# Optimization experiments

Hardware: AMD Instinct MI355X
Metric: run time of the kernel (lower is better)

Reference implementation:

```python
import jax, jax.numpy as jnp
import numpy as np

ALPHA = 0.2  # LeakyReLU negative slope
NEG_INF = -9e15


def setup_inputs() -> dict:
    key = jax.random.key(0)
    k1, k2, k3, k4 = jax.random.split(key, 4)
    B, N, F_in, F_out = 8, 2048, 256, 128
    x = jax.random.normal(k1, (B, N, F_in), dtype=jnp.float32)
    adj = jax.random.randint(k2, (B, N, N), 0, 2, dtype=jnp.int32)
    # xavier-uniform-like init
    limW = float(np.sqrt(6.0 / (F_in + F_out)))
    W = jax.random.uniform(k3, (F_in, F_out), jnp.float32, -limW, limW)
    lima = float(np.sqrt(6.0 / (2 * F_out + 1)))
    a = jax.random.uniform(k4, (2 * F_out, 1), jnp.float32, -lima, lima)
    return {"x": x, "adj": adj, "W": W, "a": a}


def reference(x, adj, W, a):
    # x: [B, N, F_in], adj: [B, N, N], W: [F_in, F_out], a: [2*F_out, 1]
    F_out = W.shape[1]
    h = jnp.einsum('bnf,fo->bno', x, W)            # [B, N, F_out]
    a1 = a[:F_out, 0]                               # attends to source node i
    a2 = a[F_out:, 0]                               # attends to target node j
    f1 = h @ a1                                     # [B, N]
    f2 = h @ a2                                     # [B, N]
    # e[b,i,j] = leakyrelu(a1.h_i + a2.h_j) -- factored form of the concat trick
    e = jax.nn.leaky_relu(f1[:, :, None] + f2[:, None, :], negative_slope=ALPHA)
    attention = jnp.where(adj > 0, e, NEG_INF)
    attention = jax.nn.softmax(attention, axis=2)   # [B, N, N]
    # dropout is identity in eval mode
    h_prime = jnp.einsum('bij,bjo->bio', attention, h)  # [B, N, F_out]
    return jax.nn.elu(h_prime)                      # concat=True -> ELU
```

## Files before the change

### kernel.cpp

```cpp
#include <hip/hip_runtime.h>
#include <stdint.h>

#define BB   8
#define NN   2048
#define FIN  256
#define FOUT 128

using short8 = __attribute__((ext_vector_type(8))) short;
using f32x4  = __attribute__((ext_vector_type(4))) float;

__device__ __forceinline__ unsigned short rbf(float f) {
    return (unsigned short)((__float_as_uint(f) + 0x8000u) >> 16);
}

__device__ __forceinline__ void mfma_calib(int m, int quad, int* Mlab, int* Nlab) {
    short8 pa1, pb1, pa2, pb2;
    const short one = (short)0x3F80;
    const short mb  = (short)rbf((float)m);
#pragma unroll
    for (int j = 0; j < 8; ++j) { pa1[j] = 0; pa2[j] = 0; pb1[j] = mb; pb2[j] = one; }
    if (quad == 0) { pa1[0] = one; pa2[0] = mb; }
    f32x4 zz = {0.f, 0.f, 0.f, 0.f};
    f32x4 c1 = __builtin_amdgcn_mfma_f32_16x16x32_bf16(pa1, pb1, zz, 0, 0, 0);
    f32x4 c2 = __builtin_amdgcn_mfma_f32_16x16x32_bf16(pa2, pb2, zz, 0, 0, 0);
#pragma unroll
    for (int r = 0; r < 4; ++r) {
        Nlab[r] = ((int)c1[r]) & 15;
        Mlab[r] = ((int)c2[r]) & 15;
    }
}

__global__ __launch_bounds__(256) void gat_wt(const float* __restrict__ W,
                                              unsigned short* __restrict__ wt) {
    const int g  = blockIdx.x * 256 + threadIdx.x;
    const int k  = g >> 5;
    const int o4 = (g & 31) << 2;
    float4 wv = *(const float4*)(W + (k << 7) + o4);
    wt[((o4 + 0) << 8) + k] = rbf(wv.x);
    wt[((o4 + 1) << 8) + k] = rbf(wv.y);
    wt[((o4 + 2) << 8) + k] = rbf(wv.z);
    wt[((o4 + 3) << 8) + k] = rbf(wv.w);
}

__global__ __launch_bounds__(256) void gat_bm2(const int* __restrict__ adj,
                                               unsigned char* __restrict__ bm) {
    const int row = blockIdx.x;
    const int tid = threadIdx.x;
    const int4* p = (const int4*)(adj + ((size_t)row << 11) + (tid << 3));
    int4 a0 = p[0];
    int4 a1 = p[1];
    unsigned int b = (unsigned int)(a0.x > 0)
                   | ((unsigned int)(a0.y > 0) << 1)
                   | ((unsigned int)(a0.z > 0) << 2)
                   | ((unsigned int)(a0.w > 0) << 3)
                   | ((unsigned int)(a1.x > 0) << 4)
                   | ((unsigned int)(a1.y > 0) << 5)
                   | ((unsigned int)(a1.z > 0) << 6)
                   | ((unsigned int)(a1.w > 0) << 7);
    const int w = tid >> 6, c = (tid >> 2) & 15, q = tid & 3;
    bm[((size_t)(row >> 5) << 13) + (c << 9) + (w << 7) + (q << 5) + (row & 31)]
        = (unsigned char)b;
}

__global__ __launch_bounds__(256) void gat_h4(
        const float* __restrict__ x, const unsigned short* __restrict__ wt,
        const float* __restrict__ a, unsigned short* __restrict__ ht,
        float* __restrict__ f1, float* __restrict__ f2) {
    __shared__ unsigned short xs[16][264];
    __shared__ float hs[16][132];
    const int bk   = blockIdx.x;
    const int R0   = bk << 4;
    const int b    = R0 >> 11;
    const int il0  = R0 & (NN - 1);
    const int tid  = threadIdx.x;
    const int w    = tid >> 6;
    const int lane = tid & 63;
    const int m    = lane & 15;
    const int quad = lane >> 4;

#pragma unroll
    for (int rr = 0; rr < 4; ++rr) {
        const int row = (w << 2) + rr;
        float4 xv = *(const float4*)(x + (size_t)(R0 + row) * FIN + (lane << 2));
        ushort4 c4;
        c4.x = rbf(xv.x); c4.y = rbf(xv.y); c4.z = rbf(xv.z); c4.w = rbf(xv.w);
        *(ushort4*)(&xs[row][lane << 2]) = c4;
    }
    int Mlab[4], Nlab[4];
    mfma_calib(m, quad, Mlab, Nlab);
    __syncthreads();

    f32x4 zz = {0.f, 0.f, 0.f, 0.f};
    f32x4 acc[2] = {zz, zz};
#pragma unroll
    for (int kc = 0; kc < 8; ++kc) {
        const int k0 = (kc << 5) + (quad << 3);
        short8 av = *(const short8*)(&xs[m][k0]);
#pragma unroll
        for (int t = 0; t < 2; ++t) {
            const int ot = (w << 1) + t;
            short8 bw = *(const short8*)(wt + (((ot << 4) + m) << 8) + k0);
            acc[t] = __builtin_amdgcn_mfma_f32_16x16x32_bf16(av, bw, acc[t], 0, 0, 0);
        }
    }
#pragma unroll
    for (int t = 0; t < 2; ++t)
#pragma unroll
        for (int r = 0; r < 4; ++r)
            hs[Mlab[r]][(((w << 1) + t) << 4) + Nlab[r]] = acc[t][r];
    __syncthreads();

    {
        const int i   = tid >> 4;
        const int seg = tid & 15;
        const int o0  = seg << 3;
        float s1 = 0.f, s2 = 0.f;
#pragma unroll
        for (int e = 0; e < 8; ++e) {
            float hv = hs[i][o0 + e];
            s1 = fmaf(hv, a[o0 + e], s1);
            s2 = fmaf(hv, a[FOUT + o0 + e], s2);
        }
        s1 += __shfl_xor(s1, 1); s1 += __shfl_xor(s1, 2);
        s1 += __shfl_xor(s1, 4); s1 += __shfl_xor(s1, 8);
        s2 += __shfl_xor(s2, 1); s2 += __shfl_xor(s2, 2);
        s2 += __shfl_xor(s2, 4); s2 += __shfl_xor(s2, 8);
        if (seg == 0) { f1[R0 + i] = s1; f2[R0 + i] = s2; }
    }
    {
        const int o  = tid >> 1;
        const int i8 = (tid & 1) << 3;
        const int jj = il0 + i8;
        const int wj = jj >> 9;
        const int cj = (jj >> 5) & 15;
        const int qj = (jj >> 3) & 3;
        short8 hv;
#pragma unroll
        for (int e = 0; e < 8; ++e) hv[e] = (short)rbf(hs[i8 + e][o]);
        const size_t addr = ((size_t)b << 18) + ((size_t)wj << 16) + (cj << 12)
                          + ((o >> 4) << 9) + (((qj << 4) + (o & 15)) << 3);
        *(short8*)(ht + addr) = hv;
    }
}

#define LOADC(H, MskA, MskB, Fa, Fb, c) { \
    const unsigned short* hp_ = htb + ((c) << 12); \
    _Pragma("unroll") \
    for (int ot = 0; ot < 8; ++ot) \
        H[ot] = *(const short8*)(hp_ + (ot << 9) + (lane << 3)); \
    MskA = bmb[((c) << 9) + mq]; \
    MskB = bmb[((c) << 9) + mq + 16]; \
    const int j0_ = jb + ((c) << 5); \
    Fa = *(const float4*)(f2b + j0_); \
    Fb = *(const float4*)(f2b + j0_ + 4); \
}

#define COMPC(H, MskA, MskB, Fa, Fb) { \
    float fm_[8] = {Fa.x, Fa.y, Fa.z, Fa.w, Fb.x, Fb.y, Fb.z, Fb.w}; \
    float pA_[8], pB_[8]; \
    _Pragma("unroll") \
    for (int u = 0; u < 8; ++u) { \
        float e = f1a + fm_[u]; \
        pA_[u] = (MskA & (1u << u)) ? __expf(fmaxf(e, 0.2f * e)) : 0.f; \
    } \
    _Pragma("unroll") \
    for (int u = 0; u < 8; ++u) { \
        float e = f1b + fm_[u]; \
        pB_[u] = (MskB & (1u << u)) ? __expf(fmaxf(e, 0.2f * e)) : 0.f; \
    } \
    s1 += ((pA_[0]+pA_[1])+(pA_[2]+pA_[3]))+((pA_[4]+pA_[5])+(pA_[6]+pA_[7])); \
    s2 += ((pB_[0]+pB_[1])+(pB_[2]+pB_[3]))+((pB_[4]+pB_[5])+(pB_[6]+pB_[7])); \
    short8 pf1_, pf2_; \
    _Pragma("unroll") \
    for (int u = 0; u < 8; ++u) { pf1_[u] = (short)rbf(pA_[u]); pf2_[u] = (short)rbf(pB_[u]); } \
    _Pragma("unroll") \
    for (int ot = 0; ot < 8; ++ot) { \
        acc1[ot] = __builtin_amdgcn_mfma_f32_16x16x32_bf16(pf1_, H[ot], acc1[ot], 0, 0, 0); \
        acc2[ot] = __builtin_amdgcn_mfma_f32_16x16x32_bf16(pf2_, H[ot], acc2[ot], 0, 0, 0); \
    } \
}

__global__ __launch_bounds__(256, 2) void gat_s6(
        const unsigned char* __restrict__ bm, const unsigned short* __restrict__ ht,
        const float* __restrict__ f1, const float* __restrict__ f2,
        float* __restrict__ out) {
    const int bk   = blockIdx.x;
    const int b    = bk & 7;
    const int i0   = (bk >> 3) << 5;
    const int tid  = threadIdx.x;
    const int w    = tid >> 6;
    const int lane = tid & 63;
    const int m    = lane & 15;
    const int quad = lane >> 4;

    __shared__ float accb[2][32][128];
    __shared__ float sbuf[4][2][16];

    const int gi0 = (b << 11) + i0;
    const float f1a = f1[gi0 + m];
    const float f1b = f1[gi0 + 16 + m];
    const unsigned char* bmb = bm + ((size_t)gi0 << 8);
    const int mq = (w << 7) + (quad << 5) + m;
    const float* f2b = f2 + (b << 11);
    const unsigned short* htb = ht + ((size_t)b << 18) + ((size_t)w << 16);

    const int jb  = (w << 9) + (quad << 3);

    f32x4 zz = {0.f, 0.f, 0.f, 0.f};
    f32x4 acc1[8], acc2[8];
#pragma unroll
    for (int t = 0; t < 8; ++t) { acc1[t] = zz; acc2[t] = zz; }
    float s1 = 0.f, s2 = 0.f;

    short8 hfA[8], hfB[8];
    unsigned int mA0, mB0, mA1, mB1;
    float4 faA, fbA, faB, fbB;

    LOADC(hfA, mA0, mB0, faA, fbA, 0);
    for (int cc = 0; cc < 7; ++cc) {
        const int c0 = cc << 1;
        LOADC(hfB, mA1, mB1, faB, fbB, c0 + 1);
        COMPC(hfA, mA0, mB0, faA, fbA);
        LOADC(hfA, mA0, mB0, faA, fbA, c0 + 2);
        COMPC(hfB, mA1, mB1, faB, fbB);
    }
    LOADC(hfB, mA1, mB1, faB, fbB, 15);
    COMPC(hfA, mA0, mB0, faA, fbA);
    COMPC(hfB, mA1, mB1, faB, fbB);

    s1 += __shfl_xor(s1, 16); s1 += __shfl_xor(s1, 32);
    s2 += __shfl_xor(s2, 16); s2 += __shfl_xor(s2, 32);
    if (lane < 16) { sbuf[w][0][lane] = s1; sbuf[w][1][lane] = s2; }

    int Mlab[4], Nlab[4];
    mfma_calib(m, quad, Mlab, Nlab);

    if (w < 2) {
#pragma unroll
        for (int ot = 0; ot < 8; ++ot)
#pragma unroll
            for (int r = 0; r < 4; ++r) {
                accb[w][Mlab[r]][(ot << 4) + Nlab[r]]      = acc1[ot][r];
                accb[w][16 + Mlab[r]][(ot << 4) + Nlab[r]] = acc2[ot][r];
            }
    }
    __syncthreads();
    if (w >= 2) {
#pragma unroll
        for (int ot = 0; ot < 8; ++ot)
#pragma unroll
            for (int r = 0; r < 4; ++r) {
                accb[w - 2][Mlab[r]][(ot << 4) + Nlab[r]]      += acc1[ot][r];
                accb[w - 2][16 + Mlab[r]][(ot << 4) + Nlab[r]] += acc2[ot][r];
            }
    }
    __syncthreads();

    {
        const int row = tid >> 3;
        const int o0  = (tid & 7) << 4;
        const int g   = row >> 4;
        const int mm  = row & 15;
        const float s = (sbuf[0][g][mm] + sbuf[1][g][mm]) +
                        (sbuf[2][g][mm] + sbuf[3][g][mm]);
        const float inv = 1.0f / s;
        float* orow = out + (((size_t)gi0 + row) << 7) + o0;
#pragma unroll
        for (int v4 = 0; v4 < 4; ++v4) {
            float4 rv;
            float y;
            y = (accb[0][row][o0 + 4 * v4 + 0] + accb[1][row][o0 + 4 * v4 + 0]) * inv;
            rv.x = y > 0.f ? y : expm1f(y);
            y = (accb[0][row][o0 + 4 * v4 + 1] + accb[1][row][o0 + 4 * v4 + 1]) * inv;
            rv.y = y > 0.f ? y : expm1f(y);
            y = (accb[0][row][o0 + 4 * v4 + 2] + accb[1][row][o0 + 4 * v4 + 2]) * inv;
            rv.z = y > 0.f ? y : expm1f(y);
            y = (accb[0][row][o0 + 4 * v4 + 3] + accb[1][row][o0 + 4 * v4 + 3]) * inv;
            rv.w = y > 0.f ? y : expm1f(y);
            *(float4*)(orow + 4 * v4) = rv;
        }
    }
}

extern "C" void kernel_launch(void* const* d_in, const int* in_sizes, int n_in,
                              void* d_out, int out_size, void* d_ws, size_t ws_size,
                              hipStream_t stream) {
    const float* x   = nullptr;
    const int*   adj = nullptr;
    const float* W   = nullptr;
    const float* a   = nullptr;
    for (int i = 0; i < n_in; ++i) {
        const long s = in_sizes[i];
        if      (s == (long)BB * NN * NN)  adj = (const int*)d_in[i];
        else if (s == (long)BB * NN * FIN) x   = (const float*)d_in[i];
        else if (s == (long)FIN * FOUT)    W   = (const float*)d_in[i];
        else if (s == 2L * FOUT)           a   = (const float*)d_in[i];
    }
    if (!x)   x   = (const float*)d_in[0];
    if (!adj) adj = (const int*)d_in[1];
    if (!W)   W   = (const float*)d_in[2];
    if (!a)   a   = (const float*)d_in[3];
    float* out = (float*)d_out;

    unsigned short* wt = (unsigned short*)d_ws;
    unsigned short* ht = wt + 32768;
    float* f1  = (float*)(ht + (size_t)BB * NN * FOUT);
    float* f2  = f1 + BB * NN;
    unsigned char* bmw = (unsigned char*)(f2 + BB * NN);

    hipLaunchKernelGGL(gat_wt,  dim3(32),    dim3(256), 0, stream, W, wt);
    hipLaunchKernelGGL(gat_bm2, dim3(16384), dim3(256), 0, stream, adj, bmw);
    hipLaunchKernelGGL(gat_h4,  dim3(1024),  dim3(256), 0, stream, x, wt, a, ht, f1, f2);
    hipLaunchKernelGGL(gat_s6,  dim3(512),   dim3(256), 0, stream, bmw, ht, f1, f2, out);
}
```

Measured before the change: 239.8 us.

## Stage adjacency bitmask writes through LDS and triple-buffer attention loads

The bitmask kernel now handles 32 rows per block. Each block packs the bits into a shared-memory tile and writes it out as coalesced 16-byte stores, replacing scattered single-byte global writes. The attention kernel moves from double to triple register buffering of the h/mask/f2 chunk loads, so loads are issued two chunks ahead of compute, and it reorders the loads within each chunk. The deeper prefetch raises register pressure under launch bounds (256,2), which risks spills, and the bitmask kernel now runs fewer, longer blocks.

```diff
diff --git a/kernel.cpp b/kernel.cpp
--- a/kernel.cpp
+++ b/kernel.cpp
@@ -42,24 +42,32 @@
     wt[((o4 + 3) << 8) + k] = rbf(wv.w);
 }
 
-__global__ __launch_bounds__(256) void gat_bm2(const int* __restrict__ adj,
+__global__ __launch_bounds__(256) void gat_bm3(const int* __restrict__ adj,
                                                unsigned char* __restrict__ bm) {
-    const int row = blockIdx.x;
+    __shared__ unsigned char tile[8192];
+    const int rg  = blockIdx.x;
     const int tid = threadIdx.x;
-    const int4* p = (const int4*)(adj + ((size_t)row << 11) + (tid << 3));
-    int4 a0 = p[0];
-    int4 a1 = p[1];
-    unsigned int b = (unsigned int)(a0.x > 0)
-                   | ((unsigned int)(a0.y > 0) << 1)
-                   | ((unsigned int)(a0.z > 0) << 2)
-                   | ((unsigned int)(a0.w > 0) << 3)
-                   | ((unsigned int)(a1.x > 0) << 4)
-                   | ((unsigned int)(a1.y > 0) << 5)
-                   | ((unsigned int)(a1.z > 0) << 6)
-                   | ((unsigned int)(a1.w > 0) << 7);
     const int w = tid >> 6, c = (tid >> 2) & 15, q = tid & 3;
-    bm[((size_t)(row >> 5) << 13) + (c << 9) + (w << 7) + (q << 5) + (row & 31)]
-        = (unsigned char)b;
+    const int dst = (c << 9) + (w << 7) + (q << 5);
+    for (int rr = 0; rr < 32; ++rr) {
+        const int4* p = (const int4*)(adj + (((size_t)(rg << 5) + rr) << 11) + (tid << 3));
+        int4 a0 = p[0];
+        int4 a1 = p[1];
+        unsigned int b = (unsigned int)(a0.x > 0)
+                       | ((unsigned int)(a0.y > 0) << 1)
+                       | ((unsigned int)(a0.z > 0) << 2)
+                       | ((unsigned int)(a0.w > 0) << 3)
+                       | ((unsigned int)(a1.x > 0) << 4)
+                       | ((unsigned int)(a1.y > 0) << 5)
+                       | ((unsigned int)(a1.z > 0) << 6)
+                       | ((unsigned int)(a1.w > 0) << 7);
+        tile[dst + rr] = (unsigned char)b;
+    }
+    __syncthreads();
+    const int4* src = (const int4*)tile;
+    int4* d4 = (int4*)(bm + ((size_t)rg << 13));
+    d4[tid]       = src[tid];
+    d4[tid + 256] = src[tid + 256];
 }
 
 __global__ __launch_bounds__(256) void gat_h4(
@@ -144,15 +152,15 @@
 }
 
 #define LOADC(H, MskA, MskB, Fa, Fb, c) { \
-    const unsigned short* hp_ = htb + ((c) << 12); \
-    _Pragma("unroll") \
-    for (int ot = 0; ot < 8; ++ot) \
-        H[ot] = *(const short8*)(hp_ + (ot << 9) + (lane << 3)); \
-    MskA = bmb[((c) << 9) + mq]; \
-    MskB = bmb[((c) << 9) + mq + 16]; \
     const int j0_ = jb + ((c) << 5); \
     Fa = *(const float4*)(f2b + j0_); \
     Fb = *(const float4*)(f2b + j0_ + 4); \
+    MskA = bmb[((c) << 9) + mq]; \
+    MskB = bmb[((c) << 9) + mq + 16]; \
+    const unsigned short* hp_ = htb + ((c) << 12); \
+    _Pragma("unroll") \
+    for (int ot = 0; ot < 8; ++ot) \
+        H[ot] = *(const short8*)(hp_ + (ot << 9) + (lane << 3)); \
 }
 
 #define COMPC(H, MskA, MskB, Fa, Fb) { \
@@ -180,7 +188,7 @@
     } \
 }
 
-__global__ __launch_bounds__(256, 2) void gat_s6(
+__global__ __launch_bounds__(256, 2) void gat_s7(
         const unsigned char* __restrict__ bm, const unsigned short* __restrict__ ht,
         const float* __restrict__ f1, const float* __restrict__ f2,
         float* __restrict__ out) {
@@ -212,21 +220,27 @@
     for (int t = 0; t < 8; ++t) { acc1[t] = zz; acc2[t] = zz; }
     float s1 = 0.f, s2 = 0.f;
 
-    short8 hfA[8], hfB[8];
-    unsigned int mA0, mB0, mA1, mB1;
-    float4 faA, fbA, faB, fbB;
-
-    LOADC(hfA, mA0, mB0, faA, fbA, 0);
-    for (int cc = 0; cc < 7; ++cc) {
-        const int c0 = cc << 1;
-        LOADC(hfB, mA1, mB1, faB, fbB, c0 + 1);
-        COMPC(hfA, mA0, mB0, faA, fbA);
-        LOADC(hfA, mA0, mB0, faA, fbA, c0 + 2);
-        COMPC(hfB, mA1, mB1, faB, fbB);
-    }
-    LOADC(hfB, mA1, mB1, faB, fbB, 15);
-    COMPC(hfA, mA0, mB0, faA, fbA);
-    COMPC(hfB, mA1, mB1, faB, fbB);
+    short8 hfA[8], hfB[8], hfC[8];
+    unsigned int mAA, mBA, mAB, mBB, mAC, mBC;
+    float4 faA, fbA, faB, fbB, faC, fbC;
+
+    LOADC(hfA, mAA, mBA, faA, fbA, 0);
+    LOADC(hfB, mAB, mBB, faB, fbB, 1);
+    for (int t = 0; t < 4; ++t) {
+        const int c0 = 3 * t;
+        LOADC(hfC, mAC, mBC, faC, fbC, c0 + 2);
+        COMPC(hfA, mAA, mBA, faA, fbA);
+        LOADC(hfA, mAA, mBA, faA, fbA, c0 + 3);
+        COMPC(hfB, mAB, mBB, faB, fbB);
+        LOADC(hfB, mAB, mBB, faB, fbB, c0 + 4);
+        COMPC(hfC, mAC, mBC, faC, fbC);
+    }
+    LOADC(hfC, mAC, mBC, faC, fbC, 14);
+    COMPC(hfA, mAA, mBA, faA, fbA);
+    LOADC(hfA, mAA, mBA, faA, fbA, 15);
+    COMPC(hfB, mAB, mBB, faB, fbB);
+    COMPC(hfC, mAC, mBC, faC, fbC);
+    COMPC(hfA, mAA, mBA, faA, fbA);
 
     s1 += __shfl_xor(s1, 16); s1 += __shfl_xor(s1, 32);
     s2 += __shfl_xor(s2, 16); s2 += __shfl_xor(s2, 32);
@@ -308,8 +322,8 @@
     float* f2  = f1 + BB * NN;
     unsigned char* bmw = (unsigned char*)(f2 + BB * NN);
 
-    hipLaunchKernelGGL(gat_wt,  dim3(32),    dim3(256), 0, stream, W, wt);
-    hipLaunchKernelGGL(gat_bm2, dim3(16384), dim3(256), 0, stream, adj, bmw);
-    hipLaunchKernelGGL(gat_h4,  dim3(1024),  dim3(256), 0, stream, x, wt, a, ht, f1, f2);
-    hipLaunchKernelGGL(gat_s6,  dim3(512),   dim3(256), 0, stream, bmw, ht, f1, f2, out);
-}
+    hipLaunchKernelGGL(gat_wt,  dim3(32),   dim3(256), 0, stream, W, wt);
+    hipLaunchKernelGGL(gat_bm3, dim3(512),  dim3(256), 0, stream, adj, bmw);
+    hipLaunchKernelGGL(gat_h4,  dim3(1024), dim3(256), 0, stream, x, wt, a, ht, f1, f2);
+    hipLaunchKernelGGL(gat_s7,  dim3(512),  dim3(256), 0, stream, bmw, ht, f1, f2, out);
+}
```

New measurement: 244.7 us. +2.0%, slower.

## Split attention kernel work by output columns with async LDS-staged H loads

Applied to the files above, without the earlier changes.

Before, each wave took a quarter of the j range and all 128 output columns, and the partial accumulators were reduced across waves through shared memory. Now each wave covers all 2048 j values for a 32-column slice of the output. Its H tiles are double-buffered in LDS through global_load_lds, with explicit vmcnt waits. This removes the cross-wave reduction and block barriers and cuts accumulator registers. In exchange, each wave recomputes the exp/softmax weights for every j, so exp work rises fourfold, and it depends on hand-tuned waitcnt ordering.

```diff
diff --git a/kernel.cpp b/kernel.cpp
--- a/kernel.cpp
+++ b/kernel.cpp
@@ -143,47 +143,61 @@
     }
 }
 
-#define LOADC(H, MskA, MskB, Fa, Fb, c) { \
-    const unsigned short* hp_ = htb + ((c) << 12); \
-    _Pragma("unroll") \
-    for (int ot = 0; ot < 8; ++ot) \
-        H[ot] = *(const short8*)(hp_ + (ot << 9) + (lane << 3)); \
-    MskA = bmb[((c) << 9) + mq]; \
-    MskB = bmb[((c) << 9) + mq + 16]; \
-    const int j0_ = jb + ((c) << 5); \
-    Fa = *(const float4*)(f2b + j0_); \
-    Fb = *(const float4*)(f2b + j0_ + 4); \
-}
-
-#define COMPC(H, MskA, MskB, Fa, Fb) { \
-    float fm_[8] = {Fa.x, Fa.y, Fa.z, Fa.w, Fb.x, Fb.y, Fb.z, Fb.w}; \
+#define GLD_LDS(gsrc, ldst) \
+    __builtin_amdgcn_global_load_lds( \
+        (const __attribute__((address_space(1))) void*)(gsrc), \
+        (__attribute__((address_space(3))) void*)(ldst), 16, 0, 0)
+
+#define STAGE(c, d) { \
+    const unsigned short* src_ = htb + ((size_t)((c) >> 4) << 16) \
+        + (((c) & 15) << 12) + (ot0 << 9) + (lane << 3); \
+    GLD_LDS(src_,       &stg[w][(d)][0]); \
+    GLD_LDS(src_ + 512, &stg[w][(d)][512]); \
+}
+
+#define SCOMP(MK_A, MK_B, F_A, F_B, d) { \
+    float fm_[8] = {F_A.x, F_A.y, F_A.z, F_A.w, F_B.x, F_B.y, F_B.z, F_B.w}; \
     float pA_[8], pB_[8]; \
     _Pragma("unroll") \
     for (int u = 0; u < 8; ++u) { \
         float e = f1a + fm_[u]; \
-        pA_[u] = (MskA & (1u << u)) ? __expf(fmaxf(e, 0.2f * e)) : 0.f; \
+        pA_[u] = (MK_A & (1u << u)) ? __expf(fmaxf(e, 0.2f * e)) : 0.f; \
     } \
     _Pragma("unroll") \
     for (int u = 0; u < 8; ++u) { \
         float e = f1b + fm_[u]; \
-        pB_[u] = (MskB & (1u << u)) ? __expf(fmaxf(e, 0.2f * e)) : 0.f; \
+        pB_[u] = (MK_B & (1u << u)) ? __expf(fmaxf(e, 0.2f * e)) : 0.f; \
     } \
     s1 += ((pA_[0]+pA_[1])+(pA_[2]+pA_[3]))+((pA_[4]+pA_[5])+(pA_[6]+pA_[7])); \
     s2 += ((pB_[0]+pB_[1])+(pB_[2]+pB_[3]))+((pB_[4]+pB_[5])+(pB_[6]+pB_[7])); \
     short8 pf1_, pf2_; \
     _Pragma("unroll") \
     for (int u = 0; u < 8; ++u) { pf1_[u] = (short)rbf(pA_[u]); pf2_[u] = (short)rbf(pB_[u]); } \
-    _Pragma("unroll") \
-    for (int ot = 0; ot < 8; ++ot) { \
-        acc1[ot] = __builtin_amdgcn_mfma_f32_16x16x32_bf16(pf1_, H[ot], acc1[ot], 0, 0, 0); \
-        acc2[ot] = __builtin_amdgcn_mfma_f32_16x16x32_bf16(pf2_, H[ot], acc2[ot], 0, 0, 0); \
-    } \
-}
-
-__global__ __launch_bounds__(256, 2) void gat_s6(
+    short8 h0_ = *(const short8*)(&stg[w][(d)][lane << 3]); \
+    short8 h1_ = *(const short8*)(&stg[w][(d)][512 + (lane << 3)]); \
+    acc00 = __builtin_amdgcn_mfma_f32_16x16x32_bf16(pf1_, h0_, acc00, 0, 0, 0); \
+    acc01 = __builtin_amdgcn_mfma_f32_16x16x32_bf16(pf1_, h1_, acc01, 0, 0, 0); \
+    acc10 = __builtin_amdgcn_mfma_f32_16x16x32_bf16(pf2_, h0_, acc10, 0, 0, 0); \
+    acc11 = __builtin_amdgcn_mfma_f32_16x16x32_bf16(pf2_, h1_, acc11, 0, 0, 0); \
+}
+
+#define SBODY(c, d, MKN_A, MKN_B, FN_A, FN_B, MK_A, MK_B, F_A, F_B) { \
+    const int cn_ = ((c) + 1) & 63; \
+    STAGE(cn_, (d) ^ 1); \
+    const int mi_ = ((cn_ & 15) << 9) + ((cn_ >> 4) << 7) + mqm; \
+    MKN_A = bmb[mi_]; MKN_B = bmb[mi_ + 16]; \
+    FN_A = *(const float4*)(f2b + (cn_ << 5) + (quad << 3)); \
+    FN_B = *(const float4*)(f2b + (cn_ << 5) + (quad << 3) + 4); \
+    asm volatile("s_waitcnt vmcnt(6)" ::: "memory"); \
+    __builtin_amdgcn_sched_barrier(0); \
+    SCOMP(MK_A, MK_B, F_A, F_B, d) \
+}
+
+__global__ __launch_bounds__(256, 2) void gat_sv(
         const unsigned char* __restrict__ bm, const unsigned short* __restrict__ ht,
         const float* __restrict__ f1, const float* __restrict__ f2,
         float* __restrict__ out) {
+    __shared__ unsigned short stg[4][2][1024];
     const int bk   = blockIdx.x;
     const int b    = bk & 7;
     const int i0   = (bk >> 3) << 5;
@@ -192,92 +206,72 @@
     const int lane = tid & 63;
     const int m    = lane & 15;
     const int quad = lane >> 4;
-
-    __shared__ float accb[2][32][128];
-    __shared__ float sbuf[4][2][16];
+    const int ot0  = w << 1;
 
     const int gi0 = (b << 11) + i0;
     const float f1a = f1[gi0 + m];
     const float f1b = f1[gi0 + 16 + m];
     const unsigned char* bmb = bm + ((size_t)gi0 << 8);
-    const int mq = (w << 7) + (quad << 5) + m;
+    const int mqm = (quad << 5) + m;
     const float* f2b = f2 + (b << 11);
-    const unsigned short* htb = ht + ((size_t)b << 18) + ((size_t)w << 16);
-
-    const int jb  = (w << 9) + (quad << 3);
+    const unsigned short* htb = ht + ((size_t)b << 18);
 
     f32x4 zz = {0.f, 0.f, 0.f, 0.f};
-    f32x4 acc1[8], acc2[8];
-#pragma unroll
-    for (int t = 0; t < 8; ++t) { acc1[t] = zz; acc2[t] = zz; }
+    f32x4 acc00 = zz, acc01 = zz, acc10 = zz, acc11 = zz;
     float s1 = 0.f, s2 = 0.f;
 
-    short8 hfA[8], hfB[8];
-    unsigned int mA0, mB0, mA1, mB1;
-    float4 faA, fbA, faB, fbB;
-
-    LOADC(hfA, mA0, mB0, faA, fbA, 0);
-    for (int cc = 0; cc < 7; ++cc) {
+    unsigned int mkA0, mkB0, mkA1, mkB1;
+    float4 fA0, fB0, fA1, fB1;
+
+    STAGE(0, 0);
+    mkA0 = bmb[mqm]; mkB0 = bmb[mqm + 16];
+    fA0 = *(const float4*)(f2b + (quad << 3));
+    fB0 = *(const float4*)(f2b + (quad << 3) + 4);
+
+    for (int cc = 0; cc < 32; ++cc) {
         const int c0 = cc << 1;
-        LOADC(hfB, mA1, mB1, faB, fbB, c0 + 1);
-        COMPC(hfA, mA0, mB0, faA, fbA);
-        LOADC(hfA, mA0, mB0, faA, fbA, c0 + 2);
-        COMPC(hfB, mA1, mB1, faB, fbB);
-    }
-    LOADC(hfB, mA1, mB1, faB, fbB, 15);
-    COMPC(hfA, mA0, mB0, faA, fbA);
-    COMPC(hfB, mA1, mB1, faB, fbB);
+        SBODY(c0,     0, mkA1, mkB1, fA1, fB1, mkA0, mkB0, fA0, fB0);
+        SBODY(c0 + 1, 1, mkA0, mkB0, fA0, fB0, mkA1, mkB1, fA1, fB1);
+    }
 
     s1 += __shfl_xor(s1, 16); s1 += __shfl_xor(s1, 32);
     s2 += __shfl_xor(s2, 16); s2 += __shfl_xor(s2, 32);
-    if (lane < 16) { sbuf[w][0][lane] = s1; sbuf[w][1][lane] = s2; }
 
     int Mlab[4], Nlab[4];
     mfma_calib(m, quad, Mlab, Nlab);
 
-    if (w < 2) {
-#pragma unroll
-        for (int ot = 0; ot < 8; ++ot)
-#pragma unroll
-            for (int r = 0; r < 4; ++r) {
-                accb[w][Mlab[r]][(ot << 4) + Nlab[r]]      = acc1[ot][r];
-                accb[w][16 + Mlab[r]][(ot << 4) + Nlab[r]] = acc2[ot][r];
-            }
-    }
-    __syncthreads();
-    if (w >= 2) {
-#pragma unroll
-        for (int ot = 0; ot < 8; ++ot)
-#pragma unroll
-            for (int r = 0; r < 4; ++r) {
-                accb[w - 2][Mlab[r]][(ot << 4) + Nlab[r]]      += acc1[ot][r];
-                accb[w - 2][16 + Mlab[r]][(ot << 4) + Nlab[r]] += acc2[ot][r];
-            }
-    }
-    __syncthreads();
+    asm volatile("s_waitcnt vmcnt(0)" ::: "memory");
+    __builtin_amdgcn_sched_barrier(0);
+
+    float* tile = (float*)&stg[w][0][0];
+#pragma unroll
+    for (int r = 0; r < 4; ++r) {
+        tile[Mlab[r] * 32 + Nlab[r]]              = acc00[r];
+        tile[Mlab[r] * 32 + 16 + Nlab[r]]         = acc01[r];
+        tile[(16 + Mlab[r]) * 32 + Nlab[r]]       = acc10[r];
+        tile[(16 + Mlab[r]) * 32 + 16 + Nlab[r]]  = acc11[r];
+    }
+    asm volatile("s_waitcnt lgkmcnt(0)" ::: "memory");
+    __builtin_amdgcn_sched_barrier(0);
 
     {
-        const int row = tid >> 3;
-        const int o0  = (tid & 7) << 4;
-        const int g   = row >> 4;
-        const int mm  = row & 15;
-        const float s = (sbuf[0][g][mm] + sbuf[1][g][mm]) +
-                        (sbuf[2][g][mm] + sbuf[3][g][mm]);
-        const float inv = 1.0f / s;
-        float* orow = out + (((size_t)gi0 + row) << 7) + o0;
-#pragma unroll
-        for (int v4 = 0; v4 < 4; ++v4) {
+        const int row = lane >> 1;
+        const int ch  = (lane & 1) << 4;
+        const float v1 = __shfl(s1, row & 15);
+        const float v2 = __shfl(s2, row & 15);
+        const float sd = (row < 16) ? v1 : v2;
+        const float inv = 1.0f / sd;
+        float* orow = out + (((size_t)gi0 + row) << 7) + (w << 5) + ch;
+#pragma unroll
+        for (int v = 0; v < 4; ++v) {
+            float4 lv = *(const float4*)&tile[row * 32 + ch + (v << 2)];
             float4 rv;
             float y;
-            y = (accb[0][row][o0 + 4 * v4 + 0] + accb[1][row][o0 + 4 * v4 + 0]) * inv;
-            rv.x = y > 0.f ? y : expm1f(y);
-            y = (accb[0][row][o0 + 4 * v4 + 1] + accb[1][row][o0 + 4 * v4 + 1]) * inv;
-            rv.y = y > 0.f ? y : expm1f(y);
-            y = (accb[0][row][o0 + 4 * v4 + 2] + accb[1][row][o0 + 4 * v4 + 2]) * inv;
-            rv.z = y > 0.f ? y : expm1f(y);
-            y = (accb[0][row][o0 + 4 * v4 + 3] + accb[1][row][o0 + 4 * v4 + 3]) * inv;
-            rv.w = y > 0.f ? y : expm1f(y);
-            *(float4*)(orow + 4 * v4) = rv;
+            y = lv.x * inv; rv.x = y > 0.f ? y : expm1f(y);
+            y = lv.y * inv; rv.y = y > 0.f ? y : expm1f(y);
+            y = lv.z * inv; rv.z = y > 0.f ? y : expm1f(y);
+            y = lv.w * inv; rv.w = y > 0.f ? y : expm1f(y);
+            *(float4*)(orow + (v << 2)) = rv;
         }
     }
 }
@@ -311,5 +305,5 @@
     hipLaunchKernelGGL(gat_wt,  dim3(32),    dim3(256), 0, stream, W, wt);
     hipLaunchKernelGGL(gat_bm2, dim3(16384), dim3(256), 0, stream, adj, bmw);
     hipLaunchKernelGGL(gat_h4,  dim3(1024),  dim3(256), 0, stream, x, wt, a, ht, f1, f2);
-    hipLaunchKernelGGL(gat_s6,  dim3(512),   dim3(256), 0, stream, bmw, ht, f1, f2, out);
-}
+    hipLaunchKernelGGL(gat_sv,  dim3(512),   dim3(256), 0, stream, bmw, ht, f1, f2, out);
+}
```

New measurement: 277.1 us. 15.5% more time.
